# Performance work log

Hardware: AMD Instinct MI355X
Metric: run time of the kernel (lower is better)

The kernel has to match this reference:

```python
import jax, jax.numpy as jnp
import numpy as np

NUM_EMBEDDINGS = 1024
EMBEDDING_DIM = 128
COMMITMENT_COST = 0.25


def setup_inputs() -> dict:
    key = jax.random.key(0)
    k_in, k_cb = jax.random.split(key)
    inputs = jax.random.normal(k_in, (65536, EMBEDDING_DIM), dtype=jnp.float32)
    # torch init: uniform(-1/K, 1/K)
    codebook = jax.random.uniform(
        k_cb, (NUM_EMBEDDINGS, EMBEDDING_DIM), dtype=jnp.float32,
        minval=-1.0 / NUM_EMBEDDINGS, maxval=1.0 / NUM_EMBEDDINGS)
    return {"inputs": inputs, "codebook": codebook}


def reference(inputs, codebook):
    # inputs: [N, D], codebook: [K, D]
    # squared euclidean distances [N, K]
    distances = (jnp.sum(inputs ** 2, axis=1, keepdims=True)
                 + jnp.sum(codebook ** 2, axis=1)
                 - 2.0 * jnp.matmul(inputs, codebook.T))
    encoding_indices = jnp.argmin(distances, axis=1)  # [N]
    encodings = jax.nn.one_hot(encoding_indices, NUM_EMBEDDINGS, dtype=jnp.float32)  # [N, K]
    # onehot @ codebook == gather
    quantized = jnp.take(codebook, encoding_indices, axis=0)  # [N, D]

    e_latent_loss = jnp.mean((jax.lax.stop_gradient(quantized) - inputs) ** 2)
    q_latent_loss = jnp.mean((quantized - jax.lax.stop_gradient(inputs)) ** 2)
    loss = q_latent_loss + COMMITMENT_COST * e_latent_loss

    # straight-through estimator
    quantized_st = inputs + jax.lax.stop_gradient(quantized - inputs)

    avg_probs = jnp.mean(encodings, axis=0)  # [K]
    perplexity = jnp.exp(-jnp.sum(avg_probs * jnp.log(avg_probs + 1e-10)))
    return (loss, quantized_st, perplexity, encodings)
```

## Files before the change

### kernel.cpp

```cpp
#include <hip/hip_runtime.h>

#define NROWS 65536
#define DIM   128
#define KC    1024
#define QST_OFF  1
#define PPL_OFF  8388609
#define ENC_OFF  8388610

typedef float floatx4 __attribute__((ext_vector_type(4)));
typedef _Float16 half8_t __attribute__((ext_vector_type(8)));
typedef _Float16 half4_t __attribute__((ext_vector_type(4)));

#define BSTR 144
#define CIMG 4608
#define CCH  9216
#define A_LO 9216
#define RPB 64

__device__ __forceinline__ float fadd_rn_(float a, float b) {
#pragma clang fp contract(off)
  return a + b;
}
__device__ __forceinline__ float fsub_rn_(float a, float b) {
#pragma clang fp contract(off)
  return a - b;
}
__device__ __forceinline__ float fmul_rn_(float a, float b) {
#pragma clang fp contract(off)
  return a * b;
}

__device__ __forceinline__ void async_ld16(const void* g, void* l) {
  __builtin_amdgcn_global_load_lds(
      (const __attribute__((address_space(1))) void*)g,
      (__attribute__((address_space(3))) void*)l, 16, 0, 0);
}

__device__ __forceinline__ float rowsq128(const float4* src) {
  float r[8];
  {
    float4 v0 = src[0], v1 = src[1];
    r[0] = fmul_rn_(v0.x, v0.x); r[1] = fmul_rn_(v0.y, v0.y);
    r[2] = fmul_rn_(v0.z, v0.z); r[3] = fmul_rn_(v0.w, v0.w);
    r[4] = fmul_rn_(v1.x, v1.x); r[5] = fmul_rn_(v1.y, v1.y);
    r[6] = fmul_rn_(v1.z, v1.z); r[7] = fmul_rn_(v1.w, v1.w);
  }
  for (int i = 1; i < 16; ++i) {
    float4 v0 = src[2 * i], v1 = src[2 * i + 1];
    r[0] = fadd_rn_(r[0], fmul_rn_(v0.x, v0.x));
    r[1] = fadd_rn_(r[1], fmul_rn_(v0.y, v0.y));
    r[2] = fadd_rn_(r[2], fmul_rn_(v0.z, v0.z));
    r[3] = fadd_rn_(r[3], fmul_rn_(v0.w, v0.w));
    r[4] = fadd_rn_(r[4], fmul_rn_(v1.x, v1.x));
    r[5] = fadd_rn_(r[5], fmul_rn_(v1.y, v1.y));
    r[6] = fadd_rn_(r[6], fmul_rn_(v1.z, v1.z));
    r[7] = fadd_rn_(r[7], fmul_rn_(v1.w, v1.w));
  }
  return fadd_rn_(fadd_rn_(fadd_rn_(r[0], r[1]), fadd_rn_(r[2], r[3])),
                  fadd_rn_(fadd_rn_(r[4], r[5]), fadd_rn_(r[6], r[7])));
}

__global__ __launch_bounds__(256) void k_prep(const float* __restrict__ cb,
                                              float* __restrict__ cbT,
                                              float* __restrict__ cc,
                                              _Float16* __restrict__ Bp) {
  __shared__ float tile[64 * 129];
  int t = threadIdx.x;
  int c0 = blockIdx.x * 64;
#pragma unroll
  for (int it = 0; it < 32; ++it) {
    int f = it * 256 + t;
    int c = f >> 7, d = f & 127;
    tile[c * 129 + d] = cb[(size_t)(c0 + c) * DIM + d];
  }
  __syncthreads();
#pragma unroll
  for (int it = 0; it < 32; ++it) {
    int f = it * 256 + t;
    int d = f >> 6, c = f & 63;
    cbT[(size_t)d * KC + c0 + c] = tile[c * 129 + d];
  }
  if (t < 64) {
    const float* s = &tile[t * 129];
    float r[8];
#pragma unroll
    for (int j = 0; j < 8; ++j) r[j] = fmul_rn_(s[j], s[j]);
    for (int i = 1; i < 16; ++i) {
#pragma unroll
      for (int j = 0; j < 8; ++j)
        r[j] = fadd_rn_(r[j], fmul_rn_(s[i * 8 + j], s[i * 8 + j]));
    }
    float ccv = fadd_rn_(fadd_rn_(fadd_rn_(r[0], r[1]), fadd_rn_(r[2], r[3])),
                         fadd_rn_(fadd_rn_(r[4], r[5]), fadd_rn_(r[6], r[7])));
    cc[c0 + t] = ccv;
    int g = c0 + t;
    size_t base = (size_t)(g >> 5) * CCH + (size_t)(g & 31) * BSTR;
#pragma unroll
    for (int k = 128; k < 144; ++k) {
      Bp[base + k] = (_Float16)0.0f;
      Bp[base + CIMG + k] = (_Float16)0.0f;
    }
    Bp[base + 128] = (_Float16)(-512.0f * ccv);
  }
#pragma unroll
  for (int it = 0; it < 32; ++it) {
    int f = it * 256 + t;
    int c = f >> 7, k = f & 127;
    int g = c0 + c;
    size_t base = (size_t)(g >> 5) * CCH + (size_t)(g & 31) * BSTR;
    float c5 = tile[c * 129 + k] * 512.0f;
    _Float16 h = (_Float16)c5;
    _Float16 l = (_Float16)(c5 - (float)h);
    Bp[base + k] = h;
    Bp[base + CIMG + k] = l;
  }
}

__global__ __launch_bounds__(256, 4) void k_main(const float* __restrict__ inp,
                                                 const float* __restrict__ cb,
                                                 const float* __restrict__ cbT,
                                                 const _Float16* __restrict__ Bp,
                                                 const float* __restrict__ cc,
                                                 float* __restrict__ out_qst,
                                                 float* __restrict__ out_enc,
                                                 int* __restrict__ cnt,
                                                 float* __restrict__ lsum) {
  __shared__ _Float16 SB[2 * CCH];
  __shared__ float xxs[RPB];
  __shared__ int bk[RPB];
  __shared__ int fl_rows[RPB];
  __shared__ int fl_cnt;
  __shared__ float xs[128];
  __shared__ float redd[4];
  __shared__ int redi[4];
  __shared__ float redf[4];
  __shared__ float mb1[RPB][2];
  __shared__ float mb2[RPB][2];
  __shared__ int mi1[RPB][2];

  int t = threadIdx.x;
  int lane = t & 63, w = t >> 6;
  int q = lane >> 4, col = lane & 15;
  int half = w & 1;
  int wrow = (w >> 1) * 32;
  int row0 = blockIdx.x * RPB;
  if (t == 0) fl_cnt = 0;

  {
    const float* src = inp + (size_t)row0 * DIM;
#pragma unroll
    for (int it = 0; it < 8; ++it) {
      int f = it * 256 + t;
      int r = f >> 5, c4 = f & 31;
      float4 v = *(const float4*)(src + (size_t)r * DIM + c4 * 4);
      _Float16 h0 = (_Float16)v.x, h1 = (_Float16)v.y, h2 = (_Float16)v.z, h3 = (_Float16)v.w;
      half4_t hv = {h0, h1, h2, h3};
      half4_t lv = {(_Float16)(v.x - (float)h0), (_Float16)(v.y - (float)h1),
                    (_Float16)(v.z - (float)h2), (_Float16)(v.w - (float)h3)};
      *(half4_t*)&SB[r * BSTR + c4 * 4] = hv;
      *(half4_t*)&SB[A_LO + r * BSTR + c4 * 4] = lv;
    }
  }
  if (t < RPB) xxs[t] = rowsq128((const float4*)(inp + (size_t)(row0 + t) * DIM));
  __syncthreads();

  int arow0 = wrow + col;
  int arow1 = arow0 + 16;
  half8_t ah0[4], al0[4], ah1[4], al1[4];
#pragma unroll
  for (int ks = 0; ks < 4; ++ks) {
    ah0[ks] = *(const half8_t*)&SB[arow0 * BSTR + ks * 32 + q * 8];
    al0[ks] = *(const half8_t*)&SB[A_LO + arow0 * BSTR + ks * 32 + q * 8];
    ah1[ks] = *(const half8_t*)&SB[arow1 * BSTR + ks * 32 + q * 8];
    al1[ks] = *(const half8_t*)&SB[A_LO + arow1 * BSTR + ks * 32 + q * 8];
  }
  __syncthreads();

  half8_t aex = {0, 0, 0, 0, 0, 0, 0, 0};
  if (q == 0) aex[0] = (_Float16)0.5f;

  float b1[8], b2[8];
  int i1[8];
#pragma unroll
  for (int j = 0; j < 8; ++j) { b1[j] = -3.4e38f; b2[j] = -3.4e38f; i1[j] = 0; }

  const float4* bp4 = (const float4*)Bp;
  floatx4* enc4 = (floatx4*)(out_enc + (size_t)row0 * KC);

  {
    const float4* gsrc = bp4;
#pragma unroll
    for (int r = 0; r < 4; ++r)
      async_ld16(gsrc + r * 256 + t, &SB[(size_t)(r * 256 + t) * 8]);
    if (t < 128) async_ld16(gsrc + 1024 + t, &SB[(size_t)(1024 + t) * 8]);
  }
  asm volatile("s_waitcnt vmcnt(0)" ::: "memory");
  __builtin_amdgcn_sched_barrier(0);
  __builtin_amdgcn_s_barrier();
  __builtin_amdgcn_sched_barrier(0);

  for (int c = 0; c < 32; ++c) {
    if (c > 0) {
      asm volatile("s_waitcnt vmcnt(2)" ::: "memory");
      __builtin_amdgcn_sched_barrier(0);
      __builtin_amdgcn_s_barrier();
      __builtin_amdgcn_sched_barrier(0);
    }
    if (c < 31) {
      const float4* gsrc = bp4 + (size_t)(c + 1) * 1152;
      int boff = ((c + 1) & 1) * CCH;
#pragma unroll
      for (int r = 0; r < 4; ++r)
        async_ld16(gsrc + r * 256 + t, &SB[boff + (size_t)(r * 256 + t) * 8]);
      if (t < 128) async_ld16(gsrc + 1024 + t, &SB[boff + (size_t)(1024 + t) * 8]);
    }
    __builtin_amdgcn_sched_barrier(0);
    {
      floatx4 z = {0.f, 0.f, 0.f, 0.f};
      __builtin_nontemporal_store(z, enc4 + (size_t)c * 512 + t);
      __builtin_nontemporal_store(z, enc4 + (size_t)c * 512 + 256 + t);
    }
    __builtin_amdgcn_sched_barrier(0);

    const _Float16* Bb = &SB[(c & 1) * CCH];
    floatx4 acc0 = (floatx4){0.f, 0.f, 0.f, 0.f};
    floatx4 acc1 = (floatx4){0.f, 0.f, 0.f, 0.f};
    int brow = half * 16 + col;

#pragma unroll
    for (int ks = 0; ks < 4; ++ks) {
      const _Float16* p = &Bb[brow * BSTR + ks * 32 + q * 8];
      half8_t bh = *(const half8_t*)p;
      half8_t bl = *(const half8_t*)(p + CIMG);
      acc0 = __builtin_amdgcn_mfma_f32_16x16x32_f16(ah0[ks], bh, acc0, 0, 0, 0);
      acc0 = __builtin_amdgcn_mfma_f32_16x16x32_f16(ah0[ks], bl, acc0, 0, 0, 0);
      acc0 = __builtin_amdgcn_mfma_f32_16x16x32_f16(al0[ks], bh, acc0, 0, 0, 0);
      acc1 = __builtin_amdgcn_mfma_f32_16x16x32_f16(ah1[ks], bh, acc1, 0, 0, 0);
      acc1 = __builtin_amdgcn_mfma_f32_16x16x32_f16(ah1[ks], bl, acc1, 0, 0, 0);
      acc1 = __builtin_amdgcn_mfma_f32_16x16x32_f16(al1[ks], bh, acc1, 0, 0, 0);
    }
    {
      half8_t bex = *(const half8_t*)&Bb[brow * BSTR + 128];
      acc0 = __builtin_amdgcn_mfma_f32_16x16x32_f16(aex, bex, acc0, 0, 0, 0);
      acc1 = __builtin_amdgcn_mfma_f32_16x16x32_f16(aex, bex, acc1, 0, 0, 0);
    }

    int kidx = c * 32 + half * 16 + col;
#pragma unroll
    for (int r = 0; r < 4; ++r) {
      {
        float s = acc0[r];
        bool gt = s > b1[r];
        b2[r] = gt ? b1[r] : fmaxf(b2[r], s);
        i1[r] = gt ? kidx : i1[r];
        b1[r] = gt ? s : b1[r];
      }
      {
        float s = acc1[r];
        bool gt = s > b1[4 + r];
        b2[4 + r] = gt ? b1[4 + r] : fmaxf(b2[4 + r], s);
        i1[4 + r] = gt ? kidx : i1[4 + r];
        b1[4 + r] = gt ? s : b1[4 + r];
      }
    }
  }

#pragma unroll
  for (int j = 0; j < 8; ++j) {
    float v1 = b1[j], v2 = b2[j];
    int ii = i1[j];
    for (int off = 1; off < 16; off <<= 1) {
      float ov1 = __shfl_xor(v1, off);
      float ov2 = __shfl_xor(v2, off);
      int oi = __shfl_xor(ii, off);
      float nb1 = fmaxf(v1, ov1);
      float nb2 = fmaxf(fminf(v1, ov1), fmaxf(v2, ov2));
      ii = (ov1 > v1) ? oi : ((ov1 < v1) ? ii : min(ii, oi));
      v1 = nb1; v2 = nb2;
    }
    b1[j] = v1; b2[j] = v2; i1[j] = ii;
  }

  if (col == 0) {
#pragma unroll
    for (int s = 0; s < 2; ++s) {
#pragma unroll
      for (int r = 0; r < 4; ++r) {
        int j = s * 4 + r;
        int row = wrow + s * 16 + q * 4 + r;
        mb1[row][half] = b1[j];
        mb2[row][half] = b2[j];
        mi1[row][half] = i1[j];
      }
    }
  }
  __syncthreads();

  if (t < RPB) {
    float a1 = mb1[t][0], a2 = mb2[t][0];
    int ai = mi1[t][0];
    float c1 = mb1[t][1], c2 = mb2[t][1];
    int ci = mi1[t][1];
    float v1 = fmaxf(a1, c1);
    float v2 = fmaxf(fminf(a1, c1), fmaxf(a2, c2));
    int ii = (c1 > a1) ? ci : ((c1 < a1) ? ai : min(ai, ci));
    bk[t] = ii;
    float dist1 = fsub_rn_(xxs[t], fmul_rn_(v1, 0.00390625f));
    float u = (dist1 >= 256.f) ? 9.4e-5f : 4.7e-5f;
    if (v1 - v2 < u * 256.0f) {
      int p = atomicAdd(&fl_cnt, 1);
      fl_rows[p] = t;
    }
  }
  __syncthreads();

  int nf = fl_cnt;
  for (int f = 0; f < nf; ++f) {
    int row = fl_rows[f];
    if (t < 128) xs[t] = inp[(size_t)(row0 + row) * DIM + t];
    __syncthreads();
    float xxr = xxs[row];
    int c0 = t * 4;
    float a0 = 0.f, a1 = 0.f, a2 = 0.f, a3 = 0.f;
    for (int d = 0; d < 128; ++d) {
      float xd = xs[d];
      float4 cv = *(const float4*)&cbT[(size_t)d * KC + c0];
      a0 = __builtin_fmaf(xd, cv.x, a0);
      a1 = __builtin_fmaf(xd, cv.y, a1);
      a2 = __builtin_fmaf(xd, cv.z, a2);
      a3 = __builtin_fmaf(xd, cv.w, a3);
    }
    float aa[4] = {a0, a1, a2, a3};
    float bb = 3.4e38f;
    int bi = 0;
#pragma unroll
    for (int j = 0; j < 4; ++j) {
      float dist = fsub_rn_(fadd_rn_(xxr, cc[c0 + j]), fmul_rn_(2.0f, aa[j]));
      if (dist < bb) { bb = dist; bi = c0 + j; }
    }
    for (int off = 1; off < 64; off <<= 1) {
      float ov = __shfl_xor(bb, off);
      int oi = __shfl_xor(bi, off);
      if (ov < bb || (ov == bb && oi < bi)) { bb = ov; bi = oi; }
    }
    if (lane == 0) { redd[w] = bb; redi[w] = bi; }
    __syncthreads();
    if (t == 0) {
      float vb = redd[0];
      int ib = redi[0];
#pragma unroll
      for (int ww = 1; ww < 4; ++ww) {
        if (redd[ww] < vb || (redd[ww] == vb && redi[ww] < ib)) { vb = redd[ww]; ib = redi[ww]; }
      }
      bk[row] = ib;
    }
    __syncthreads();
  }

  if (t < RPB) atomicAdd(&cnt[bk[t]], 1);

  float ls = 0.f;
#pragma unroll 4
  for (int it = 0; it < 32; ++it) {
    int f = it * 256 + t;
    int row = f >> 7, d = f & 127;
    size_t gro = (size_t)(row0 + row) * DIM + d;
    float x = inp[gro];
    float qv = cb[(size_t)bk[row] * DIM + d];
    float qe = fsub_rn_(qv, x);
    __builtin_nontemporal_store(fadd_rn_(x, qe), &out_qst[gro]);
    ls = __builtin_fmaf(qe, qe, ls);
  }

  if (t < RPB) out_enc[(size_t)(row0 + t) * KC + bk[t]] = 1.0f;

  for (int off = 32; off; off >>= 1) ls += __shfl_down(ls, off);
  if (lane == 0) redf[w] = ls;
  __syncthreads();
  if (t == 0) atomicAdd(lsum, redf[0] + redf[1] + redf[2] + redf[3]);
}

__global__ __launch_bounds__(1024) void k_scalars(const int* __restrict__ cnt,
                                                  const float* __restrict__ lsum,
                                                  float* __restrict__ out) {
  int t = threadIdx.x;
  float p = (float)cnt[t] * (1.0f / 65536.0f);
  float term = fmul_rn_(p, logf(fadd_rn_(p, 1e-10f)));
  for (int off = 32; off; off >>= 1) term += __shfl_down(term, off);
  __shared__ float red[16];
  if ((t & 63) == 0) red[t >> 6] = term;
  __syncthreads();
  if (t == 0) {
    float s = 0.f;
#pragma unroll
    for (int w = 0; w < 16; ++w) s += red[w];
    out[PPL_OFF] = expf(-s);
    float e = *lsum * (1.0f / 8388608.0f);
    out[0] = fadd_rn_(e, fmul_rn_(0.25f, e));
  }
}

extern "C" void kernel_launch(void* const* d_in, const int* in_sizes, int n_in,
                              void* d_out, int out_size, void* d_ws, size_t ws_size,
                              hipStream_t stream) {
  const float* inp = (const float*)d_in[0];
  const float* cb = (const float*)d_in[1];
  float* out = (float*)d_out;

  _Float16* Bp = (_Float16*)d_ws;
  float* cbT = (float*)(Bp + 32 * CCH);
  float* cc = cbT + DIM * KC;
  int* cnt = (int*)(cc + KC);
  float* lsum = (float*)(cnt + KC);

  (void)hipMemsetAsync(cnt, 0, (KC + 1) * sizeof(int), stream);
  k_prep<<<KC / 64, 256, 0, stream>>>(cb, cbT, cc, Bp);
  k_main<<<NROWS / RPB, 256, 0, stream>>>(inp, cb, cbT, Bp, cc,
                                          out + QST_OFF, out + ENC_OFF, cnt, lsum);
  k_scalars<<<1, 1024, 0, stream>>>(cnt, lsum, out);
}
```

Baseline: 389.8 us.

## Move encodings zero-fill and counter reset from main kernel into prep kernel

The prep kernel now launches one block per 64-row tile. Each block zero-fills its slice of the one-hot encodings output with nontemporal stores, and one block clears the histogram counters, which removes the separate memset launch. The main kernel no longer interleaves zero stores with its MFMA loop, and its hand-tuned vmcnt waits plus raw barriers are replaced by a plain __syncthreads per chunk. This removes write traffic that competed with the codebook prefetch inside the main loop. In exchange, the large zero-fill becomes a serialized pass before the main kernel instead of overlapping with compute, and the simpler barrier may wait on more outstanding memory operations.

```diff
diff --git a/kernel.cpp b/kernel.cpp
--- a/kernel.cpp
+++ b/kernel.cpp
@@ -63,56 +63,73 @@
 __global__ __launch_bounds__(256) void k_prep(const float* __restrict__ cb,
                                               float* __restrict__ cbT,
                                               float* __restrict__ cc,
-                                              _Float16* __restrict__ Bp) {
+                                              _Float16* __restrict__ Bp,
+                                              float* __restrict__ enc,
+                                              int* __restrict__ cnti) {
   __shared__ float tile[64 * 129];
   int t = threadIdx.x;
-  int c0 = blockIdx.x * 64;
-#pragma unroll
-  for (int it = 0; it < 32; ++it) {
-    int f = it * 256 + t;
-    int c = f >> 7, d = f & 127;
-    tile[c * 129 + d] = cb[(size_t)(c0 + c) * DIM + d];
-  }
-  __syncthreads();
-#pragma unroll
-  for (int it = 0; it < 32; ++it) {
-    int f = it * 256 + t;
-    int d = f >> 6, c = f & 63;
-    cbT[(size_t)d * KC + c0 + c] = tile[c * 129 + d];
-  }
-  if (t < 64) {
-    const float* s = &tile[t * 129];
-    float r[8];
-#pragma unroll
-    for (int j = 0; j < 8; ++j) r[j] = fmul_rn_(s[j], s[j]);
-    for (int i = 1; i < 16; ++i) {
-#pragma unroll
-      for (int j = 0; j < 8; ++j)
-        r[j] = fadd_rn_(r[j], fmul_rn_(s[i * 8 + j], s[i * 8 + j]));
-    }
-    float ccv = fadd_rn_(fadd_rn_(fadd_rn_(r[0], r[1]), fadd_rn_(r[2], r[3])),
-                         fadd_rn_(fadd_rn_(r[4], r[5]), fadd_rn_(r[6], r[7])));
-    cc[c0 + t] = ccv;
-    int g = c0 + t;
-    size_t base = (size_t)(g >> 5) * CCH + (size_t)(g & 31) * BSTR;
-#pragma unroll
-    for (int k = 128; k < 144; ++k) {
-      Bp[base + k] = (_Float16)0.0f;
-      Bp[base + CIMG + k] = (_Float16)0.0f;
-    }
-    Bp[base + 128] = (_Float16)(-512.0f * ccv);
-  }
-#pragma unroll
-  for (int it = 0; it < 32; ++it) {
-    int f = it * 256 + t;
-    int c = f >> 7, k = f & 127;
-    int g = c0 + c;
-    size_t base = (size_t)(g >> 5) * CCH + (size_t)(g & 31) * BSTR;
-    float c5 = tile[c * 129 + k] * 512.0f;
-    _Float16 h = (_Float16)c5;
-    _Float16 l = (_Float16)(c5 - (float)h);
-    Bp[base + k] = h;
-    Bp[base + CIMG + k] = l;
+  int bid = blockIdx.x;
+
+  if (bid < 16) {
+    int c0 = bid * 64;
+#pragma unroll
+    for (int it = 0; it < 32; ++it) {
+      int f = it * 256 + t;
+      int c = f >> 7, d = f & 127;
+      tile[c * 129 + d] = cb[(size_t)(c0 + c) * DIM + d];
+    }
+    __syncthreads();
+#pragma unroll
+    for (int it = 0; it < 32; ++it) {
+      int f = it * 256 + t;
+      int d = f >> 6, c = f & 63;
+      cbT[(size_t)d * KC + c0 + c] = tile[c * 129 + d];
+    }
+    if (t < 64) {
+      const float* s = &tile[t * 129];
+      float r[8];
+#pragma unroll
+      for (int j = 0; j < 8; ++j) r[j] = fmul_rn_(s[j], s[j]);
+      for (int i = 1; i < 16; ++i) {
+#pragma unroll
+        for (int j = 0; j < 8; ++j)
+          r[j] = fadd_rn_(r[j], fmul_rn_(s[i * 8 + j], s[i * 8 + j]));
+      }
+      float ccv = fadd_rn_(fadd_rn_(fadd_rn_(r[0], r[1]), fadd_rn_(r[2], r[3])),
+                           fadd_rn_(fadd_rn_(r[4], r[5]), fadd_rn_(r[6], r[7])));
+      cc[c0 + t] = ccv;
+      int g = c0 + t;
+      size_t base = (size_t)(g >> 5) * CCH + (size_t)(g & 31) * BSTR;
+#pragma unroll
+      for (int k = 128; k < 144; ++k) {
+        Bp[base + k] = (_Float16)0.0f;
+        Bp[base + CIMG + k] = (_Float16)0.0f;
+      }
+      Bp[base + 128] = (_Float16)(-512.0f * ccv);
+    }
+#pragma unroll
+    for (int it = 0; it < 32; ++it) {
+      int f = it * 256 + t;
+      int c = f >> 7, k = f & 127;
+      int g = c0 + c;
+      size_t base = (size_t)(g >> 5) * CCH + (size_t)(g & 31) * BSTR;
+      float c5 = tile[c * 129 + k] * 512.0f;
+      _Float16 h = (_Float16)c5;
+      _Float16 l = (_Float16)(c5 - (float)h);
+      Bp[base + k] = h;
+      Bp[base + CIMG + k] = l;
+    }
+  }
+
+  {
+    floatx4 z = {0.f, 0.f, 0.f, 0.f};
+    floatx4* e4 = (floatx4*)(enc + (size_t)bid * RPB * KC);
+#pragma unroll 4
+    for (int i = 0; i < 64; ++i)
+      __builtin_nontemporal_store(z, e4 + i * 256 + t);
+  }
+  if (bid == 16) {
+    for (int i = t; i < KC + 1; i += 256) cnti[i] = 0;
   }
 }
 
@@ -185,7 +202,6 @@
   for (int j = 0; j < 8; ++j) { b1[j] = -3.4e38f; b2[j] = -3.4e38f; i1[j] = 0; }
 
   const float4* bp4 = (const float4*)Bp;
-  floatx4* enc4 = (floatx4*)(out_enc + (size_t)row0 * KC);
 
   {
     const float4* gsrc = bp4;
@@ -194,18 +210,9 @@
       async_ld16(gsrc + r * 256 + t, &SB[(size_t)(r * 256 + t) * 8]);
     if (t < 128) async_ld16(gsrc + 1024 + t, &SB[(size_t)(1024 + t) * 8]);
   }
-  asm volatile("s_waitcnt vmcnt(0)" ::: "memory");
-  __builtin_amdgcn_sched_barrier(0);
-  __builtin_amdgcn_s_barrier();
-  __builtin_amdgcn_sched_barrier(0);
 
   for (int c = 0; c < 32; ++c) {
-    if (c > 0) {
-      asm volatile("s_waitcnt vmcnt(2)" ::: "memory");
-      __builtin_amdgcn_sched_barrier(0);
-      __builtin_amdgcn_s_barrier();
-      __builtin_amdgcn_sched_barrier(0);
-    }
+    __syncthreads();
     if (c < 31) {
       const float4* gsrc = bp4 + (size_t)(c + 1) * 1152;
       int boff = ((c + 1) & 1) * CCH;
@@ -214,13 +221,6 @@
         async_ld16(gsrc + r * 256 + t, &SB[boff + (size_t)(r * 256 + t) * 8]);
       if (t < 128) async_ld16(gsrc + 1024 + t, &SB[boff + (size_t)(1024 + t) * 8]);
     }
-    __builtin_amdgcn_sched_barrier(0);
-    {
-      floatx4 z = {0.f, 0.f, 0.f, 0.f};
-      __builtin_nontemporal_store(z, enc4 + (size_t)c * 512 + t);
-      __builtin_nontemporal_store(z, enc4 + (size_t)c * 512 + 256 + t);
-    }
-    __builtin_amdgcn_sched_barrier(0);
 
     const _Float16* Bb = &SB[(c & 1) * CCH];
     floatx4 acc0 = (floatx4){0.f, 0.f, 0.f, 0.f};
@@ -413,8 +413,7 @@
   int* cnt = (int*)(cc + KC);
   float* lsum = (float*)(cnt + KC);
 
-  (void)hipMemsetAsync(cnt, 0, (KC + 1) * sizeof(int), stream);
-  k_prep<<<KC / 64, 256, 0, stream>>>(cb, cbT, cc, Bp);
+  k_prep<<<NROWS / RPB, 256, 0, stream>>>(cb, cbT, cc, Bp, out + ENC_OFF, cnt);
   k_main<<<NROWS / RPB, 256, 0, stream>>>(inp, cb, cbT, Bp, cc,
                                           out + QST_OFF, out + ENC_OFF, cnt, lsum);
   k_scalars<<<1, 1024, 0, stream>>>(cnt, lsum, out);
```

Result: slower. 431.5 us (+10.7%).
